# Kernel optimization log

Hardware: AMD Instinct MI355X
Metric: run time of the kernel (lower is better)

## Reference

```python
import jax, jax.numpy as jnp
import numpy as np
from jax import lax

EPS = 1e-5
NUM_BITS = 8          # activation quantization bits
NUM_BITS_WEIGHT = 8   # weight quantization bits


def fake_quant(x, bits):
    """Uniform min-max quantize-dequantize (per-tensor), STE on round."""
    mn = jnp.min(x)
    mx = jnp.max(x)
    scale = jnp.maximum((mx - mn) / (2 ** bits - 1), jnp.asarray(1e-8, x.dtype))
    q = jnp.round((x - mn) / scale) * scale + mn
    # straight-through estimator: identity gradient through rounding
    return x + lax.stop_gradient(q - x)


def batchnorm(x, gamma, beta, mean, var):
    # x: [N, C, H, W]; stats per channel C (eval mode, running stats)
    inv = gamma / jnp.sqrt(var + EPS)
    return x * inv[None, :, None, None] + (beta - mean * inv)[None, :, None, None]


def qconv(x, w, padding):
    xq = fake_quant(x, NUM_BITS)
    wq = fake_quant(w, NUM_BITS_WEIGHT)
    return lax.conv_general_dilated(
        xq, wq, window_strides=(1, 1), padding=padding,
        dimension_numbers=("NCHW", "OIHW", "NCHW"))


def setup_inputs() -> dict:
    key = jax.random.key(0)
    ks = jax.random.split(key, 8)
    C_in, bn_size, growth = 512, 4, 32
    C_mid = bn_size * growth  # 128
    N, H, W = 64, 28, 28
    x = jax.random.normal(ks[0], (N, C_in, H, W), dtype=jnp.float32)
    gamma1 = jax.random.uniform(ks[1], (C_in,), minval=0.5, maxval=1.5)
    beta1 = jax.random.normal(ks[2], (C_in,)) * 0.1
    mean1 = jax.random.normal(ks[3], (C_in,)) * 0.1
    var1 = jax.random.uniform(ks[4], (C_in,), minval=0.5, maxval=1.5)
    w1 = jax.random.normal(ks[5], (C_mid, C_in, 1, 1)) * (1.0 / np.sqrt(C_in))
    gamma2 = jax.random.uniform(ks[6], (C_mid,), minval=0.5, maxval=1.5)
    beta2 = jax.random.normal(ks[7], (C_mid,)) * 0.1
    mean2 = jax.random.normal(jax.random.fold_in(key, 10), (C_mid,)) * 0.1
    var2 = jax.random.uniform(jax.random.fold_in(key, 11), (C_mid,), minval=0.5, maxval=1.5)
    w2 = jax.random.normal(jax.random.fold_in(key, 12), (growth, C_mid, 3, 3)) * (1.0 / np.sqrt(C_mid * 9))
    return {"x": x, "gamma1": gamma1, "beta1": beta1, "mean1": mean1, "var1": var1,
            "w1": w1, "gamma2": gamma2, "beta2": beta2, "mean2": mean2, "var2": var2,
            "w2": w2}


def reference(x, gamma1, beta1, mean1, var1, w1, gamma2, beta2, mean2, var2, w2):
    h = jax.nn.relu(batchnorm(x, gamma1, beta1, mean1, var1))
    h = qconv(h, w1, padding=((0, 0), (0, 0)))            # 1x1 conv, 512 -> 128
    h = jax.nn.relu(batchnorm(h, gamma2, beta2, mean2, var2))
    h = qconv(h, w2, padding=((1, 1), (1, 1)))            # 3x3 conv, 128 -> 32
    # drop_rate == 0 -> dropout is identity
    return h
```

## Files before the change

### kernel.cpp

```cpp
#include <hip/hip_runtime.h>

typedef unsigned short u16;
typedef unsigned short u16x4 __attribute__((ext_vector_type(4)));
typedef unsigned short u16x8 __attribute__((ext_vector_type(8)));
typedef short bf16x8 __attribute__((ext_vector_type(8)));
typedef float f32x4 __attribute__((ext_vector_type(4)));

#define EPSF 1e-5f

#define NB   64
#define C1   512
#define C2   128
#define C3   32
#define HH   28
#define WW   28
#define HW   784
#define NHW  50176
#define XELEMS 25690112
#define K1_BLOCKS 2048
#define CONV1_BLOCKS 392
#define CONV2_BLOCKS 784

#define WS_BN1I   64
#define WS_BN1B   2112
#define WS_BN2I   4160
#define WS_BN2B   4672
#define WS_WQ1    5376
#define WS_WQ2    136448
#define WS_P1     210176
#define WS_P2     226560
#define WS_PW1    232832
#define WS_PW2    233344
#define WS_H2     233472

__device__ __forceinline__ float bf2f(u16 u) { return __uint_as_float(((unsigned)u) << 16); }
__device__ __forceinline__ u16 f2bf(float f) {
  unsigned x = __float_as_uint(f);
  return (u16)((x + 0x7fffu + ((x >> 16) & 1u)) >> 16);
}
__device__ __forceinline__ float finz(float f) {
  unsigned u = __float_as_uint(f);
  return ((u & 0x7f800000u) == 0x7f800000u) ? 0.0f : f;
}

__device__ __forceinline__ void block_minmax(float& mn, float& mx) {
  for (int m = 32; m; m >>= 1) {
    mn = fminf(mn, __shfl_xor(mn, m));
    mx = fmaxf(mx, __shfl_xor(mx, m));
  }
  __shared__ float wmn[4], wmx[4];
  const int wv = threadIdx.x >> 6;
  if ((threadIdx.x & 63) == 0) { wmn[wv] = mn; wmx[wv] = mx; }
  __syncthreads();
  if (threadIdx.x == 0) {
    mn = fminf(fminf(wmn[0], wmn[1]), fminf(wmn[2], wmn[3]));
    mx = fmaxf(fmaxf(wmx[0], wmx[1]), fmaxf(wmx[2], wmx[3]));
  }
}

__global__ __launch_bounds__(256) void kwA_kernel(const float* g1, const float* be1,
                                                  const float* m1, const float* v1,
                                                  const float* w1,
                                                  const float* g2, const float* be2,
                                                  const float* m2, const float* v2,
                                                  const float* w2, unsigned char* ws) {
  const int t = threadIdx.x;
  const int b = blockIdx.x;
  float2* pw1 = (float2*)(ws + WS_PW1);
  float2* pw2 = (float2*)(ws + WS_PW2);

  if (b == 80) {
    float* bn1i = (float*)(ws + WS_BN1I);
    float* bn1b = (float*)(ws + WS_BN1B);
    float* bn2i = (float*)(ws + WS_BN2I);
    float* bn2b = (float*)(ws + WS_BN2B);
    for (int c = t; c < C1; c += 256) {
      float inv = g1[c] / sqrtf(v1[c] + EPSF);
      bn1i[c] = inv;
      bn1b[c] = be1[c] - m1[c] * inv;
    }
    if (t < C2) {
      float inv = g2[t] / sqrtf(v2[t] + EPSF);
      bn2i[t] = inv;
      bn2b[t] = be2[t] - m2[t] * inv;
    }
    return;
  }

  float mn = 3.4e38f, mx = -3.4e38f;
  if (b < 64) {
    f32x4 v = *(const f32x4*)(w1 + b * 1024 + t * 4);
#pragma unroll
    for (int j = 0; j < 4; j++) {
      float f = finz(v[j]); mn = fminf(mn, f); mx = fmaxf(mx, f);
    }
    block_minmax(mn, mx);
    if (t == 0) pw1[b] = make_float2(mn, mx);
  } else {
    const int base = (b - 64) * 2304;
#pragma unroll
    for (int j = 0; j < 9; j++) {
      float f = finz(w2[base + t + j * 256]); mn = fminf(mn, f); mx = fmaxf(mx, f);
    }
    block_minmax(mn, mx);
    if (t == 0) pw2[b - 64] = make_float2(mn, mx);
  }
}

__global__ __launch_bounds__(256) void kwB_kernel(const float* w1, const float* w2,
                                                  unsigned char* ws) {
  const float2* pw1 = (const float2*)(ws + WS_PW1);
  const float2* pw2 = (const float2*)(ws + WS_PW2);
  u16* wq1 = (u16*)(ws + WS_WQ1);
  u16* wq2 = (u16*)(ws + WS_WQ2);
  const int t = threadIdx.x;
  const int b = blockIdx.x;
  __shared__ float bc[2];

  if (b < 64) {
    if (t < 64) {
      float2 p = pw1[t];
      float mn = p.x, mx = p.y;
      for (int m = 32; m; m >>= 1) {
        mn = fminf(mn, __shfl_xor(mn, m));
        mx = fmaxf(mx, __shfl_xor(mx, m));
      }
      if (t == 0) { bc[0] = mn; bc[1] = mx; }
    }
    __syncthreads();
    const float mn = bc[0];
    const float s = fmaxf((bc[1] - mn) / 255.0f, 1e-8f);
    const float rs = 1.0f / s;
    f32x4 v = *(const f32x4*)(w1 + b * 1024 + t * 4);
    u16x4 o;
#pragma unroll
    for (int j = 0; j < 4; j++)
      o[j] = f2bf(fmaf(rintf((finz(v[j]) - mn) * rs), s, mn));
    *(u16x4*)(wq1 + b * 1024 + t * 4) = o;
  } else {
    if (t < 64) {
      float2 p = (t < 16) ? pw2[t] : make_float2(3.4e38f, -3.4e38f);
      float mn = p.x, mx = p.y;
      for (int m = 32; m; m >>= 1) {
        mn = fminf(mn, __shfl_xor(mn, m));
        mx = fmaxf(mx, __shfl_xor(mx, m));
      }
      if (t == 0) { bc[0] = mn; bc[1] = mx; }
    }
    __syncthreads();
    const float mn = bc[0];
    const float s = fmaxf((bc[1] - mn) / 255.0f, 1e-8f);
    const float rs = 1.0f / s;
    const int base = (b - 64) * 2304;
#pragma unroll
    for (int j = 0; j < 9; j++) {
      int o = base + t + j * 256;
      int tap = o >> 12;
      int rem = o & 4095;
      float f = finz(w2[rem * 9 + tap]);
      wq2[o] = f2bf(fmaf(rintf((f - mn) * rs), s, mn));
    }
  }
}

__global__ __launch_bounds__(256) void k1_minmax(const float* __restrict__ x, unsigned char* ws) {
  const float* bn1i = (const float*)(ws + WS_BN1I);
  const float* bn1b = (const float*)(ws + WS_BN1B);
  float2* p1 = (float2*)(ws + WS_P1);
  int gid = blockIdx.x * blockDim.x + threadIdx.x;
  int stride = gridDim.x * blockDim.x;
  const int ngroups = XELEMS / 4;
  float mn = 3.4e38f, mx = 0.0f;
  for (int i = gid; i < ngroups; i += stride) {
    int base = i * 4;
    int c = (base / HW) & (C1 - 1);
    float inv = bn1i[c], bb = bn1b[c];
    f32x4 u = *((const f32x4*)x + i);
#pragma unroll
    for (int j = 0; j < 4; j++) {
      float f = fmaxf(fmaf(u[j], inv, bb), 0.0f);
      mn = fminf(mn, f); mx = fmaxf(mx, f);
    }
  }
  block_minmax(mn, mx);
  if (threadIdx.x == 0) p1[blockIdx.x] = make_float2(mn, mx);
}

__global__ __launch_bounds__(256) void conv1_kernel(const float* __restrict__ x,
                                                    unsigned char* ws) {
  const float* bn1i = (const float*)(ws + WS_BN1I);
  const float* bn1b = (const float*)(ws + WS_BN1B);
  const float* bn2i = (const float*)(ws + WS_BN2I);
  const float* bn2b = (const float*)(ws + WS_BN2B);
  const u16* wq1 = (const u16*)(ws + WS_WQ1);
  const float2* p1 = (const float2*)(ws + WS_P1);
  float2* p2 = (float2*)(ws + WS_P2);
  u16* h2 = (u16*)(ws + WS_H2);

  __shared__ __align__(16) u16 Alds[2][128 * 40];
  __shared__ __align__(16) u16 Blds[2][128 * 40];
  __shared__ float bc[2];
  __shared__ float wred[8];

  const int t = threadIdx.x;
  const int sp0 = blockIdx.x * 128;

  {
    float* rmn = (float*)&Alds[0][0];
    float* rmx = (float*)&Blds[0][0];
    const f32x4* p4 = (const f32x4*)p1;
    float mn = 3.4e38f, mx = 0.0f;
#pragma unroll
    for (int i = 0; i < 4; i++) {
      f32x4 v = p4[t + i * 256];
      mn = fminf(mn, fminf(v[0], v[2]));
      mx = fmaxf(mx, fmaxf(v[1], v[3]));
    }
    rmn[t] = mn; rmx[t] = mx;
    __syncthreads();
    for (int s = 128; s > 0; s >>= 1) {
      if (t < s) { rmn[t] = fminf(rmn[t], rmn[t + s]); rmx[t] = fmaxf(rmx[t], rmx[t + s]); }
      __syncthreads();
    }
    if (t == 0) { bc[0] = rmn[0]; bc[1] = rmx[0]; }
    __syncthreads();
  }
  const float mn1 = bc[0];
  const float s1 = fmaxf((bc[1] - mn1) / 255.0f, 1e-8f);
  const float r1 = 1.0f / s1;

  const int kk = t >> 3;
  const int spA = (t & 7) * 8;
  const int spB = 64 + spA;
  const int ga = sp0 + spA, gb = sp0 + spB;
  const int na = ga / HW, hwa = ga % HW;
  const int nb = gb / HW, hwb = gb % HW;
  const float* xA = x + na * (C1 * HW) + hwa;
  const float* xB = x + nb * (C1 * HW) + hwb;
  const int colg = (kk & 7) + 8 * ((((kk >> 3) + (spA >> 3))) & 3);

  const int wco = t >> 1;
  const int wko = (t & 1) * 16;
  const int ab0 = wko >> 3;
  const int aswz = (wco >> 3) & 3;

  const int lane = t & 63;
  const int l15 = lane & 15;
  const int q = lane >> 4;
  const int wv = t >> 6;
  const int wy = wv >> 1;
  const int wx = wv & 1;

  f32x4 acc[4][4] = {};

  u16x8 a0 = *(const u16x8*)(wq1 + wco * C1 + wko);
  u16x8 a1 = *(const u16x8*)(wq1 + wco * C1 + wko + 8);
  f32x4 va0 = *(const f32x4*)(xA + kk * HW);
  f32x4 va1 = *(const f32x4*)(xA + kk * HW + 4);
  f32x4 vb0 = *(const f32x4*)(xB + kk * HW);
  f32x4 vb1 = *(const f32x4*)(xB + kk * HW + 4);
  float inv = bn1i[kk], bb = bn1b[kk];

#pragma unroll 1
  for (int i = 0; i < 16; i++) {
    const int cur = i & 1;
    *(u16x8*)&Alds[cur][wco * 40 + (((ab0 + 0 + aswz) & 3) << 3)] = a0;
    *(u16x8*)&Alds[cur][wco * 40 + (((ab0 + 1 + aswz) & 3) << 3)] = a1;
#pragma unroll
    for (int j = 0; j < 4; j++) {
      float f0 = fmaxf(fmaf(va0[j], inv, bb), 0.0f);
      Blds[cur][(spA + j) * 40 + colg] = f2bf(fmaf(rintf((f0 - mn1) * r1), s1, mn1));
      float f1 = fmaxf(fmaf(va1[j], inv, bb), 0.0f);
      Blds[cur][(spA + 4 + j) * 40 + colg] = f2bf(fmaf(rintf((f1 - mn1) * r1), s1, mn1));
      float g0 = fmaxf(fmaf(vb0[j], inv, bb), 0.0f);
      Blds[cur][(spB + j) * 40 + colg] = f2bf(fmaf(rintf((g0 - mn1) * r1), s1, mn1));
      float g1v = fmaxf(fmaf(vb1[j], inv, bb), 0.0f);
      Blds[cur][(spB + 4 + j) * 40 + colg] = f2bf(fmaf(rintf((g1v - mn1) * r1), s1, mn1));
    }
    if (i < 15) {
      const int kn = (i + 1) * 32;
      a0 = *(const u16x8*)(wq1 + wco * C1 + kn + wko);
      a1 = *(const u16x8*)(wq1 + wco * C1 + kn + wko + 8);
      const int c = kn + kk;
      va0 = *(const f32x4*)(xA + c * HW);
      va1 = *(const f32x4*)(xA + c * HW + 4);
      vb0 = *(const f32x4*)(xB + c * HW);
      vb1 = *(const f32x4*)(xB + c * HW + 4);
      inv = bn1i[c]; bb = bn1b[c];
    }
    __syncthreads();
    bf16x8 af[4], bfr[4];
#pragma unroll
    for (int ii = 0; ii < 4; ii++) {
      int R = wy * 64 + ii * 16 + l15;
      af[ii] = *(const bf16x8*)&Alds[cur][R * 40 + (((q + (R >> 3)) & 3) << 3)];
    }
#pragma unroll
    for (int j = 0; j < 4; j++) {
      int R = wx * 64 + j * 16 + l15;
      bfr[j] = *(const bf16x8*)&Blds[cur][R * 40 + (((q + (R >> 3)) & 3) << 3)];
    }
#pragma unroll
    for (int ii = 0; ii < 4; ii++)
#pragma unroll
      for (int j = 0; j < 4; j++)
        acc[ii][j] = __builtin_amdgcn_mfma_f32_16x16x32_bf16(af[ii], bfr[j], acc[ii][j], 0, 0, 0);
  }

  float lmn = 3.4e38f, lmx = 0.0f;
#pragma unroll
  for (int i = 0; i < 4; i++) {
    int cob = wy * 64 + i * 16 + q * 4;
    f32x4 i2 = *(const f32x4*)&bn2i[cob];
    f32x4 b2 = *(const f32x4*)&bn2b[cob];
#pragma unroll
    for (int j = 0; j < 4; j++) {
      int sp = sp0 + wx * 64 + j * 16 + l15;
      u16x4 v;
#pragma unroll
      for (int r = 0; r < 4; r++) {
        float h = fmaxf(fmaf(acc[i][j][r], i2[r], b2[r]), 0.0f);
        v[r] = f2bf(h);
        lmn = fminf(lmn, h); lmx = fmaxf(lmx, h);
      }
      *(u16x4*)&h2[sp * C2 + cob] = v;
    }
  }
  for (int m = 32; m; m >>= 1) {
    lmn = fminf(lmn, __shfl_xor(lmn, m));
    lmx = fmaxf(lmx, __shfl_xor(lmx, m));
  }
  if (lane == 0) { wred[wv] = lmn; wred[4 + wv] = lmx; }
  __syncthreads();
  if (t == 0) {
    float2 pr;
    pr.x = fminf(fminf(wred[0], wred[1]), fminf(wred[2], wred[3]));
    pr.y = fmaxf(fmaxf(wred[4], wred[5]), fmaxf(wred[6], wred[7]));
    p2[blockIdx.x] = pr;
  }
}

__global__ __launch_bounds__(256) void conv2_kernel(const unsigned char* ws,
                                                    float* __restrict__ out) {
  const u16* wq2 = (const u16*)(ws + WS_WQ2);
  const u16* h2 = (const u16*)(ws + WS_H2);
  const float2* p2 = (const float2*)(ws + WS_P2);
  __shared__ float bc2[2];

  const int t = threadIdx.x;
  {
    float mn = 3.4e38f, mx = 0.0f;
    for (int i = t; i < CONV1_BLOCKS; i += 256) {
      float2 p = p2[i];
      mn = fminf(mn, p.x); mx = fmaxf(mx, p.y);
    }
    block_minmax(mn, mx);
    if (t == 0) { bc2[0] = mn; bc2[1] = mx; }
    __syncthreads();
  }
  const float mn2 = bc2[0];
  const float s2 = fmaxf((bc2[1] - mn2) / 255.0f, 1e-8f);
  const float r2 = 1.0f / s2;

  const int lane = t & 63;
  const int l15 = lane & 15;
  const int q = lane >> 4;
  const int wv = t >> 6;

  const int B = blockIdx.x;
  const int sblk = (B & 7) * 98 + (B >> 3);
  const int spf = sblk * 64 + wv * 16 + l15;
  const int nn = spf / HW;
  const int hwf = spf % HW;
  const int hf = hwf / WW;
  const int wf = hwf % WW;

  f32x4 acc[2] = {};
  bf16x8 bz;
#pragma unroll
  for (int j = 0; j < 8; j++) bz[j] = 0;

  for (int tap = 0; tap < 9; tap++) {
    const int dh = tap / 3 - 1, dw = tap % 3 - 1;
    const u16* wA = wq2 + tap * (C3 * C2);
    unsigned h2i = (unsigned)(hf + dh);
    unsigned w2i = (unsigned)(wf + dw);
    const bool val = (h2i < 28u) && (w2i < 28u);
    const u16* bptr = h2 + ((size_t)(nn * HW + (int)h2i * WW + (int)w2i)) * C2;
#pragma unroll
    for (int ks = 0; ks < C2; ks += 32) {
      bf16x8 a[2], b;
#pragma unroll
      for (int f = 0; f < 2; f++)
        a[f] = *(const bf16x8*)(wA + (f * 16 + l15) * C2 + ks + q * 8);
      if (val) {
        u16x8 hv = *(const u16x8*)(bptr + ks + q * 8);
#pragma unroll
        for (int j = 0; j < 8; j++) {
          float h = bf2f(hv[j]);
          b[j] = (short)f2bf(fmaf(rintf((h - mn2) * r2), s2, mn2));
        }
      } else {
        b = bz;
      }
#pragma unroll
      for (int i = 0; i < 2; i++)
        acc[i] = __builtin_amdgcn_mfma_f32_16x16x32_bf16(a[i], b, acc[i], 0, 0, 0);
    }
  }

#pragma unroll
  for (int i = 0; i < 2; i++) {
    int co = i * 16 + q * 4;
#pragma unroll
    for (int r = 0; r < 4; r++)
      out[(nn * C3 + co + r) * HW + hwf] = acc[i][r];
  }
}

extern "C" void kernel_launch(void* const* d_in, const int* in_sizes, int n_in,
                              void* d_out, int out_size, void* d_ws, size_t ws_size,
                              hipStream_t stream) {
  const float* x  = (const float*)d_in[0];
  const float* g1 = (const float*)d_in[1];
  const float* b1 = (const float*)d_in[2];
  const float* m1 = (const float*)d_in[3];
  const float* v1 = (const float*)d_in[4];
  const float* w1 = (const float*)d_in[5];
  const float* g2 = (const float*)d_in[6];
  const float* b2 = (const float*)d_in[7];
  const float* m2 = (const float*)d_in[8];
  const float* v2 = (const float*)d_in[9];
  const float* w2 = (const float*)d_in[10];
  unsigned char* ws = (unsigned char*)d_ws;
  float* out = (float*)d_out;

  kwA_kernel<<<81, 256, 0, stream>>>(g1, b1, m1, v1, w1, g2, b2, m2, v2, w2, ws);
  kwB_kernel<<<80, 256, 0, stream>>>(w1, w2, ws);
  k1_minmax<<<K1_BLOCKS, 256, 0, stream>>>(x, ws);
  conv1_kernel<<<CONV1_BLOCKS, 256, 0, stream>>>(x, ws);
  conv2_kernel<<<CONV2_BLOCKS, 256, 0, stream>>>(ws, out);
}
```

Baseline: 248.3 us.

## Halve conv1 spatial tile and merge weight quantization kernels

The 1x1 conv kernel's spatial tile per block drops from 128 to 64 positions. That doubles the grid to 784 blocks, which should fill the GPU's compute units more evenly and shrink the accumulator register footprint. The cost is that each block reloads the full quantized weight tile for half the output work. Separately, the two weight-prep kernels become one: every block redundantly reduces the whole weight tensor's min/max, which removes a launch and the partial-result round trip at the price of repeated small weight reads.

New measurement: 258.8 us. 4.2% more time.

```diff
diff --git a/kernel.cpp b/kernel.cpp
--- a/kernel.cpp
+++ b/kernel.cpp
@@ -18,7 +18,7 @@
 #define NHW  50176
 #define XELEMS 25690112
 #define K1_BLOCKS 2048
-#define CONV1_BLOCKS 392
+#define CONV1_BLOCKS 784
 #define CONV2_BLOCKS 784
 
 #define WS_BN1I   64
@@ -29,8 +29,6 @@
 #define WS_WQ2    136448
 #define WS_P1     210176
 #define WS_P2     226560
-#define WS_PW1    232832
-#define WS_PW2    233344
 #define WS_H2     233472
 
 __device__ __forceinline__ float bf2f(u16 u) { return __uint_as_float(((unsigned)u) << 16); }
@@ -58,16 +56,17 @@
   }
 }
 
-__global__ __launch_bounds__(256) void kwA_kernel(const float* g1, const float* be1,
-                                                  const float* m1, const float* v1,
-                                                  const float* w1,
-                                                  const float* g2, const float* be2,
-                                                  const float* m2, const float* v2,
-                                                  const float* w2, unsigned char* ws) {
+__global__ __launch_bounds__(256) void kw_kernel(const float* g1, const float* be1,
+                                                 const float* m1, const float* v1,
+                                                 const float* w1,
+                                                 const float* g2, const float* be2,
+                                                 const float* m2, const float* v2,
+                                                 const float* w2, unsigned char* ws) {
   const int t = threadIdx.x;
   const int b = blockIdx.x;
-  float2* pw1 = (float2*)(ws + WS_PW1);
-  float2* pw2 = (float2*)(ws + WS_PW2);
+  u16* wq1 = (u16*)(ws + WS_WQ1);
+  u16* wq2 = (u16*)(ws + WS_WQ2);
+  __shared__ float bc[2];
 
   if (b == 80) {
     float* bn1i = (float*)(ws + WS_BN1I);
@@ -89,67 +88,42 @@
 
   float mn = 3.4e38f, mx = -3.4e38f;
   if (b < 64) {
-    f32x4 v = *(const f32x4*)(w1 + b * 1024 + t * 4);
-#pragma unroll
-    for (int j = 0; j < 4; j++) {
-      float f = finz(v[j]); mn = fminf(mn, f); mx = fmaxf(mx, f);
+    const f32x4* w4 = (const f32x4*)w1;
+#pragma unroll 4
+    for (int i = t; i < 16384; i += 256) {
+      f32x4 v = w4[i];
+#pragma unroll
+      for (int j = 0; j < 4; j++) {
+        float f = finz(v[j]); mn = fminf(mn, f); mx = fmaxf(mx, f);
+      }
     }
     block_minmax(mn, mx);
-    if (t == 0) pw1[b] = make_float2(mn, mx);
-  } else {
-    const int base = (b - 64) * 2304;
-#pragma unroll
-    for (int j = 0; j < 9; j++) {
-      float f = finz(w2[base + t + j * 256]); mn = fminf(mn, f); mx = fmaxf(mx, f);
-    }
-    block_minmax(mn, mx);
-    if (t == 0) pw2[b - 64] = make_float2(mn, mx);
-  }
-}
-
-__global__ __launch_bounds__(256) void kwB_kernel(const float* w1, const float* w2,
-                                                  unsigned char* ws) {
-  const float2* pw1 = (const float2*)(ws + WS_PW1);
-  const float2* pw2 = (const float2*)(ws + WS_PW2);
-  u16* wq1 = (u16*)(ws + WS_WQ1);
-  u16* wq2 = (u16*)(ws + WS_WQ2);
-  const int t = threadIdx.x;
-  const int b = blockIdx.x;
-  __shared__ float bc[2];
-
-  if (b < 64) {
-    if (t < 64) {
-      float2 p = pw1[t];
-      float mn = p.x, mx = p.y;
-      for (int m = 32; m; m >>= 1) {
-        mn = fminf(mn, __shfl_xor(mn, m));
-        mx = fmaxf(mx, __shfl_xor(mx, m));
-      }
-      if (t == 0) { bc[0] = mn; bc[1] = mx; }
-    }
-    __syncthreads();
-    const float mn = bc[0];
-    const float s = fmaxf((bc[1] - mn) / 255.0f, 1e-8f);
+    if (t == 0) { bc[0] = mn; bc[1] = mx; }
+    __syncthreads();
+    const float m0 = bc[0];
+    const float s = fmaxf((bc[1] - m0) / 255.0f, 1e-8f);
     const float rs = 1.0f / s;
-    f32x4 v = *(const f32x4*)(w1 + b * 1024 + t * 4);
+    f32x4 v = w4[b * 256 + t];
     u16x4 o;
 #pragma unroll
     for (int j = 0; j < 4; j++)
-      o[j] = f2bf(fmaf(rintf((finz(v[j]) - mn) * rs), s, mn));
+      o[j] = f2bf(fmaf(rintf((finz(v[j]) - m0) * rs), s, m0));
     *(u16x4*)(wq1 + b * 1024 + t * 4) = o;
   } else {
-    if (t < 64) {
-      float2 p = (t < 16) ? pw2[t] : make_float2(3.4e38f, -3.4e38f);
-      float mn = p.x, mx = p.y;
-      for (int m = 32; m; m >>= 1) {
-        mn = fminf(mn, __shfl_xor(mn, m));
-        mx = fmaxf(mx, __shfl_xor(mx, m));
+    const f32x4* w4 = (const f32x4*)w2;
+#pragma unroll 4
+    for (int i = t; i < 9216; i += 256) {
+      f32x4 v = w4[i];
+#pragma unroll
+      for (int j = 0; j < 4; j++) {
+        float f = finz(v[j]); mn = fminf(mn, f); mx = fmaxf(mx, f);
       }
-      if (t == 0) { bc[0] = mn; bc[1] = mx; }
-    }
-    __syncthreads();
-    const float mn = bc[0];
-    const float s = fmaxf((bc[1] - mn) / 255.0f, 1e-8f);
+    }
+    block_minmax(mn, mx);
+    if (t == 0) { bc[0] = mn; bc[1] = mx; }
+    __syncthreads();
+    const float m0 = bc[0];
+    const float s = fmaxf((bc[1] - m0) / 255.0f, 1e-8f);
     const float rs = 1.0f / s;
     const int base = (b - 64) * 2304;
 #pragma unroll
@@ -158,7 +132,7 @@
       int tap = o >> 12;
       int rem = o & 4095;
       float f = finz(w2[rem * 9 + tap]);
-      wq2[o] = f2bf(fmaf(rintf((f - mn) * rs), s, mn));
+      wq2[o] = f2bf(fmaf(rintf((f - m0) * rs), s, m0));
     }
   }
 }
@@ -198,16 +172,16 @@
   u16* h2 = (u16*)(ws + WS_H2);
 
   __shared__ __align__(16) u16 Alds[2][128 * 40];
-  __shared__ __align__(16) u16 Blds[2][128 * 40];
+  __shared__ __align__(16) u16 Blds[2][64 * 40];
   __shared__ float bc[2];
   __shared__ float wred[8];
 
   const int t = threadIdx.x;
-  const int sp0 = blockIdx.x * 128;
+  const int sp0 = blockIdx.x * 64;
 
   {
     float* rmn = (float*)&Alds[0][0];
-    float* rmx = (float*)&Blds[0][0];
+    float* rmx = (float*)&Alds[1][0];
     const f32x4* p4 = (const f32x4*)p1;
     float mn = 3.4e38f, mx = 0.0f;
 #pragma unroll
@@ -231,12 +205,9 @@
 
   const int kk = t >> 3;
   const int spA = (t & 7) * 8;
-  const int spB = 64 + spA;
-  const int ga = sp0 + spA, gb = sp0 + spB;
+  const int ga = sp0 + spA;
   const int na = ga / HW, hwa = ga % HW;
-  const int nb = gb / HW, hwb = gb % HW;
   const float* xA = x + na * (C1 * HW) + hwa;
-  const float* xB = x + nb * (C1 * HW) + hwb;
   const int colg = (kk & 7) + 8 * ((((kk >> 3) + (spA >> 3))) & 3);
 
   const int wco = t >> 1;
@@ -251,14 +222,12 @@
   const int wy = wv >> 1;
   const int wx = wv & 1;
 
-  f32x4 acc[4][4] = {};
+  f32x4 acc[4][2] = {};
 
   u16x8 a0 = *(const u16x8*)(wq1 + wco * C1 + wko);
   u16x8 a1 = *(const u16x8*)(wq1 + wco * C1 + wko + 8);
   f32x4 va0 = *(const f32x4*)(xA + kk * HW);
   f32x4 va1 = *(const f32x4*)(xA + kk * HW + 4);
-  f32x4 vb0 = *(const f32x4*)(xB + kk * HW);
-  f32x4 vb1 = *(const f32x4*)(xB + kk * HW + 4);
   float inv = bn1i[kk], bb = bn1b[kk];
 
 #pragma unroll 1
@@ -272,10 +241,6 @@
       Blds[cur][(spA + j) * 40 + colg] = f2bf(fmaf(rintf((f0 - mn1) * r1), s1, mn1));
       float f1 = fmaxf(fmaf(va1[j], inv, bb), 0.0f);
       Blds[cur][(spA + 4 + j) * 40 + colg] = f2bf(fmaf(rintf((f1 - mn1) * r1), s1, mn1));
-      float g0 = fmaxf(fmaf(vb0[j], inv, bb), 0.0f);
-      Blds[cur][(spB + j) * 40 + colg] = f2bf(fmaf(rintf((g0 - mn1) * r1), s1, mn1));
-      float g1v = fmaxf(fmaf(vb1[j], inv, bb), 0.0f);
-      Blds[cur][(spB + 4 + j) * 40 + colg] = f2bf(fmaf(rintf((g1v - mn1) * r1), s1, mn1));
     }
     if (i < 15) {
       const int kn = (i + 1) * 32;
@@ -284,26 +249,24 @@
       const int c = kn + kk;
       va0 = *(const f32x4*)(xA + c * HW);
       va1 = *(const f32x4*)(xA + c * HW + 4);
-      vb0 = *(const f32x4*)(xB + c * HW);
-      vb1 = *(const f32x4*)(xB + c * HW + 4);
       inv = bn1i[c]; bb = bn1b[c];
     }
     __syncthreads();
-    bf16x8 af[4], bfr[4];
+    bf16x8 af[4], bfr[2];
 #pragma unroll
     for (int ii = 0; ii < 4; ii++) {
       int R = wy * 64 + ii * 16 + l15;
       af[ii] = *(const bf16x8*)&Alds[cur][R * 40 + (((q + (R >> 3)) & 3) << 3)];
     }
 #pragma unroll
-    for (int j = 0; j < 4; j++) {
-      int R = wx * 64 + j * 16 + l15;
+    for (int j = 0; j < 2; j++) {
+      int R = wx * 32 + j * 16 + l15;
       bfr[j] = *(const bf16x8*)&Blds[cur][R * 40 + (((q + (R >> 3)) & 3) << 3)];
     }
 #pragma unroll
     for (int ii = 0; ii < 4; ii++)
 #pragma unroll
-      for (int j = 0; j < 4; j++)
+      for (int j = 0; j < 2; j++)
         acc[ii][j] = __builtin_amdgcn_mfma_f32_16x16x32_bf16(af[ii], bfr[j], acc[ii][j], 0, 0, 0);
   }
 
@@ -314,8 +277,8 @@
     f32x4 i2 = *(const f32x4*)&bn2i[cob];
     f32x4 b2 = *(const f32x4*)&bn2b[cob];
 #pragma unroll
-    for (int j = 0; j < 4; j++) {
-      int sp = sp0 + wx * 64 + j * 16 + l15;
+    for (int j = 0; j < 2; j++) {
+      int sp = sp0 + wx * 32 + j * 16 + l15;
       u16x4 v;
 #pragma unroll
       for (int r = 0; r < 4; r++) {
@@ -435,8 +398,7 @@
   unsigned char* ws = (unsigned char*)d_ws;
   float* out = (float*)d_out;
 
-  kwA_kernel<<<81, 256, 0, stream>>>(g1, b1, m1, v1, w1, g2, b2, m2, v2, w2, ws);
-  kwB_kernel<<<80, 256, 0, stream>>>(w1, w2, ws);
+  kw_kernel<<<81, 256, 0, stream>>>(g1, b1, m1, v1, w1, g2, b2, m2, v2, w2, ws);
   k1_minmax<<<K1_BLOCKS, 256, 0, stream>>>(x, ws);
   conv1_kernel<<<CONV1_BLOCKS, 256, 0, stream>>>(x, ws);
   conv2_kernel<<<CONV2_BLOCKS, 256, 0, stream>>>(ws, out);
```
